# Kernel optimization log

Hardware: AMD Instinct MI355X
Metric: run time of the kernel (lower is better)

## Reference

```python
import jax, jax.numpy as jnp
import numpy as np

EPS = 1e-6
R = 8


def _gram_schmidt(U, eps=EPS):
    # Modified Gram-Schmidt over the r columns of U (dim, r), matching the
    # sequential projection loop in HouseholderReflection.get_orthogonal_matrix.
    cols = []
    u0 = U[:, 0]
    cols.append(u0 / (jnp.linalg.norm(u0) + eps))
    r = U.shape[1]
    for i in range(1, r):
        ui = U[:, i]
        for j in range(i):
            ui = ui - jnp.dot(cols[j], ui) * cols[j]
        cols.append(ui / (jnp.linalg.norm(ui) + eps))
    return cols  # list of r unit vectors (dim,)


def _orthogonal_matrix(hra_u, eps=EPS):
    # Q = prod_i (I - 2 u_i u_i^T), applied as rank-1 updates: Q <- Q - 2 (Q u) u^T
    dim = hra_u.shape[0]
    cols = _gram_schmidt(hra_u, eps)
    Q = jnp.eye(dim, dtype=hra_u.dtype)
    for u in cols:
        Q = Q - 2.0 * jnp.outer(Q @ u, u)
    return Q  # (dim, dim)


def setup_inputs() -> dict:
    key = jax.random.key(0)
    k1, k2, k3, k4, k5 = jax.random.split(key, 5)
    N, D_IN, D_HID, D_OUT = 4096, 2048, 8192, 2048
    x = jax.random.normal(k1, (N, D_IN), dtype=jnp.float32)
    hra_u = jax.random.normal(k2, (D_IN, R), dtype=jnp.float32)
    W_random = jax.random.normal(k3, (D_IN, D_HID), dtype=jnp.float32) / np.sqrt(D_IN)
    W_out = jax.random.normal(k4, (D_HID, D_OUT), dtype=jnp.float32) / np.sqrt(D_HID)
    bias = jax.random.normal(k5, (D_OUT,), dtype=jnp.float32)
    return {"x": x, "hra_u": hra_u, "W_random": W_random, "W_out": W_out, "bias": bias}


def reference(x, hra_u, W_random, W_out, bias):
    # y = gelu(x @ (Q @ W_random)) @ W_out + bias  (torch nn.GELU = exact erf gelu)
    Q = _orthogonal_matrix(hra_u)
    W_t = Q @ W_random                      # (D_IN, D_HID)
    h = jax.nn.gelu(x @ W_t, approximate=False)  # (N, D_HID)
    return h @ W_out + bias                 # (N, D_OUT)
```

## Files before the change

### kernel.cpp

```cpp
#include <hip/hip_runtime.h>
#include <hip/hip_bf16.h>

typedef __bf16 bf16;
typedef __bf16 bf16x4 __attribute__((ext_vector_type(4)));
typedef __bf16 bf16x8 __attribute__((ext_vector_type(8)));
typedef float  f32x4  __attribute__((ext_vector_type(4)));

#define GAS __attribute__((address_space(1)))
#define LAS __attribute__((address_space(3)))

#define NROWS 4096
#define DIN   2048
#define DHID  8192
#define DOUT  2048

__device__ __forceinline__ void gload16(const void* g, void* l) {
    __builtin_amdgcn_global_load_lds((GAS void*)g, (LAS void*)l, 16, 0, 0);
}
template <int N> __device__ __forceinline__ void vmw() {
    asm volatile("s_waitcnt vmcnt(%0)" :: "n"(N));
}
__device__ __forceinline__ void SB() { __builtin_amdgcn_sched_barrier(0); }

__global__ __launch_bounds__(64) void gs_kernel(const float* __restrict__ U,
                                                float* __restrict__ Vt) {
    __shared__ float Vs[8][DIN];
    const int l = threadIdx.x;
    float u[32];
    for (int r = 0; r < 8; ++r) {
        #pragma unroll
        for (int s = 0; s < 32; ++s) u[s] = U[(size_t)(l * 32 + s) * 8 + r];
        for (int j = 0; j < r; ++j) {
            float d = 0.f;
            #pragma unroll
            for (int s = 0; s < 32; ++s) d += Vs[j][l * 32 + s] * u[s];
            #pragma unroll
            for (int o = 32; o >= 1; o >>= 1) d += __shfl_xor(d, o);
            #pragma unroll
            for (int s = 0; s < 32; ++s) u[s] -= d * Vs[j][l * 32 + s];
        }
        float nr = 0.f;
        #pragma unroll
        for (int s = 0; s < 32; ++s) nr += u[s] * u[s];
        #pragma unroll
        for (int o = 32; o >= 1; o >>= 1) nr += __shfl_xor(nr, o);
        const float inv = 1.f / (sqrtf(nr) + 1e-6f);
        #pragma unroll
        for (int s = 0; s < 32; ++s) {
            float v = u[s] * inv;
            Vs[r][l * 32 + s] = v;
            Vt[r * DIN + l * 32 + s] = v;
        }
        __syncthreads();
    }
}

__global__ __launch_bounds__(256) void p_kernel(const float* __restrict__ W,
                                                const float* __restrict__ Vt,
                                                float* __restrict__ P) {
    const int t = threadIdx.x;
    const int c = blockIdx.x * 32 + (t & 31);
    const int part = t >> 5;
    float acc[8] = {};
    const int i0 = part * 256;
    #pragma unroll 4
    for (int i = i0; i < i0 + 256; ++i) {
        float w = W[(size_t)i * DHID + c];
        #pragma unroll
        for (int r = 0; r < 8; ++r) acc[r] = fmaf(Vt[r * DIN + i], w, acc[r]);
    }
    __shared__ float red[8][8][32];
    #pragma unroll
    for (int r = 0; r < 8; ++r) red[part][r][t & 31] = acc[r];
    __syncthreads();
    {
        int r = t >> 5, cc = t & 31;
        float s = 0.f;
        #pragma unroll
        for (int p = 0; p < 8; ++p) s += red[p][r][cc];
        P[(size_t)r * DHID + blockIdx.x * 32 + cc] = s;
    }
}

__global__ __launch_bounds__(256) void xv_kernel(const float* __restrict__ x,
                                                 const float* __restrict__ Vt,
                                                 float* __restrict__ xV,
                                                 bf16* __restrict__ xb) {
    const int row = blockIdx.x * 4 + (threadIdx.x >> 6);
    const int l = threadIdx.x & 63;
    const float* xr = x + (size_t)row * DIN;
    bf16* xbr = xb + (size_t)row * DIN;
    float acc[8] = {};
    #pragma unroll
    for (int s = 0; s < 8; ++s) {
        const int c0 = (s * 64 + l) * 4;
        float4 v = *(const float4*)&xr[c0];
        bf16x4 o = { (bf16)v.x, (bf16)v.y, (bf16)v.z, (bf16)v.w };
        *(bf16x4*)&xbr[c0] = o;
        #pragma unroll
        for (int r = 0; r < 8; ++r) {
            float4 vt = *(const float4*)&Vt[r * DIN + c0];
            acc[r] = fmaf(v.x, vt.x, fmaf(v.y, vt.y, fmaf(v.z, vt.z, fmaf(v.w, vt.w, acc[r]))));
        }
    }
    #pragma unroll
    for (int r = 0; r < 8; ++r) {
        float d = acc[r];
        #pragma unroll
        for (int o = 32; o >= 1; o >>= 1) d += __shfl_xor(d, o);
        if (l == 0) xV[(size_t)row * 8 + r] = d;
    }
}

__global__ __launch_bounds__(256) void tconv_kernel(const float* __restrict__ in,
                                                    bf16* __restrict__ out,
                                                    int R, int C) {
    __shared__ bf16 tile[64][66];
    const int t = threadIdx.x;
    const int n0 = blockIdx.x * 64, k0 = blockIdx.y * 64;
    const int rr = t >> 4, c4 = (t & 15) * 4;
    #pragma unroll
    for (int q = 0; q < 4; ++q) {
        int row = k0 + rr + q * 16;
        float4 v = *(const float4*)&in[(size_t)row * C + n0 + c4];
        tile[c4 + 0][rr + q * 16] = (bf16)v.x;
        tile[c4 + 1][rr + q * 16] = (bf16)v.y;
        tile[c4 + 2][rr + q * 16] = (bf16)v.z;
        tile[c4 + 3][rr + q * 16] = (bf16)v.w;
    }
    __syncthreads();
    const int n = t >> 2, kk = (t & 3) * 16;
    unsigned int w[8];
    #pragma unroll
    for (int i = 0; i < 8; ++i) w[i] = *(const unsigned int*)&tile[n][kk + i * 2];
    uint4 lo = { w[0], w[1], w[2], w[3] }, hi = { w[4], w[5], w[6], w[7] };
    uint4* dst = (uint4*)&out[(size_t)(n0 + n) * R + k0 + kk];
    dst[0] = lo;
    dst[1] = hi;
}

__global__ __launch_bounds__(256) void redk(float* __restrict__ out,
                                            const float* __restrict__ p1,
                                            const float* __restrict__ bias) {
    const size_t i = (size_t)blockIdx.x * 256 + threadIdx.x;
    float4 a = ((const float4*)out)[i];
    float4 b = ((const float4*)p1)[i];
    const int c4 = (int)(i & (DOUT / 4 - 1)) * 4;
    float4 bb = *(const float4*)&bias[c4];
    float4 r = { a.x + b.x + bb.x, a.y + b.y + bb.y,
                 a.z + b.z + bb.z, a.w + b.w + bb.w };
    ((float4*)out)[i] = r;
}

template <int CR, int CC, int EPI>
__global__ __launch_bounds__(512) void gemm4p(const bf16* __restrict__ A,
                                              const bf16* __restrict__ Bt,
                                              const int N, const int nk, const int lda,
                                              const float* __restrict__ e0,
                                              const float* __restrict__ e1,
                                              void* __restrict__ Cout) {
    __shared__ __align__(128) char lds[131072];
    const int t = threadIdx.x;
    const int wid = t >> 6, lane = t & 63;
    const int wr = wid >> 2, wc = wid & 3;
    const int lrow = lane & 15;
    const int lk2 = (lane >> 4) * 16;

    int bid = blockIdx.x, sk = 0;
    if constexpr (EPI == 2) { sk = bid & 1; bid >>= 1; }
    const int chunks_c = (N >> 8) / CC;
    const int xc = bid & 7;
    const int ii = bid >> 3;
    const int bm = (xc / chunks_c) * CR + ii / CC;
    const int bn = (xc % chunks_c) * CC + ii % CC;

    const size_t koff = (size_t)sk * nk * 64;
    const bf16* Abase = A + (size_t)bm * 256 * lda + koff;
    const bf16* Bbase = Bt + (size_t)bn * 256 * lda + koff;

    const unsigned aswz = (unsigned)(((lrow >> 1) & 3) << 4);
    const unsigned aoff0 = (unsigned)((wr * 128 + lrow) * 64 + lk2) ^ aswz;
    const unsigned boff0 = (unsigned)((wc * 64 + lrow) * 64 + lk2) ^ aswz;

    f32x4 acc[8][4] = {};

    auto STAGEQ = [&](int kt, int q) {
        const bf16* Pb = (q < 2) ? Abase : Bbase;
        const size_t kq = (size_t)kt * 64 + (size_t)(q & 1) * 32;
        char* reg = lds + (kt & 1) * 65536 + q * 16384;
        #pragma unroll
        for (int i2 = 0; i2 < 2; ++i2) {
            const int lin = i2 * 512 + t;
            const int row = lin >> 2;
            const int g = (lin & 3) ^ ((lin >> 3) & 3);
            gload16(Pb + (size_t)row * lda + kq + g * 8,
                    reg + (i2 * 512 + (t & 448)) * 16);
        }
    };

    auto PH_SYNC = [&]() {
        SB();
        __builtin_amdgcn_s_barrier();
        asm volatile("s_waitcnt lgkmcnt(0)");
        SB();
    };

    auto TILE64 = [&](int kt, bool dostage) {
        const char* bp = lds + (kt & 1) * 65536;
        bf16x8 av[4], bv[4], aw[4], av2[4], bv2[4], aw2[4];
        #pragma unroll
        for (int m = 0; m < 4; ++m) av[m] = *(const bf16x8*)(bp + aoff0 + m * 1024);
        #pragma unroll
        for (int n = 0; n < 4; ++n) bv[n] = *(const bf16x8*)(bp + 32768 + boff0 + n * 1024);
        if (dostage) STAGEQ(kt + 1, 0);
        PH_SYNC();
        __builtin_amdgcn_s_setprio(1);
        #pragma unroll
        for (int m = 0; m < 4; ++m)
            #pragma unroll
            for (int n = 0; n < 4; ++n)
                acc[m][n] = __builtin_amdgcn_mfma_f32_16x16x32_bf16(av[m], bv[n], acc[m][n], 0, 0, 0);
        __builtin_amdgcn_s_setprio(0);
        #pragma unroll
        for (int m = 0; m < 4; ++m) aw[m] = *(const bf16x8*)(bp + aoff0 + (m + 4) * 1024);
        if (dostage) { STAGEQ(kt + 1, 2); SB(); vmw<4>(); }
        else         { SB(); vmw<0>(); }
        PH_SYNC();
        __builtin_amdgcn_s_setprio(1);
        #pragma unroll
        for (int m = 0; m < 4; ++m)
            #pragma unroll
            for (int n = 0; n < 4; ++n)
                acc[m + 4][n] = __builtin_amdgcn_mfma_f32_16x16x32_bf16(aw[m], bv[n], acc[m + 4][n], 0, 0, 0);
        __builtin_amdgcn_s_setprio(0);
        #pragma unroll
        for (int m = 0; m < 4; ++m) av2[m] = *(const bf16x8*)(bp + 16384 + aoff0 + m * 1024);
        #pragma unroll
        for (int n = 0; n < 4; ++n) bv2[n] = *(const bf16x8*)(bp + 49152 + boff0 + n * 1024);
        if (dostage) STAGEQ(kt + 1, 1);
        PH_SYNC();
        __builtin_amdgcn_s_setprio(1);
        #pragma unroll
        for (int m = 0; m < 4; ++m)
            #pragma unroll
            for (int n = 0; n < 4; ++n)
                acc[m][n] = __builtin_amdgcn_mfma_f32_16x16x32_bf16(av2[m], bv2[n], acc[m][n], 0, 0, 0);
        __builtin_amdgcn_s_setprio(0);
        #pragma unroll
        for (int m = 0; m < 4; ++m) aw2[m] = *(const bf16x8*)(bp + 16384 + aoff0 + (m + 4) * 1024);
        if (dostage) { STAGEQ(kt + 1, 3); SB(); vmw<4>(); }
        PH_SYNC();
        __builtin_amdgcn_s_setprio(1);
        #pragma unroll
        for (int m = 0; m < 4; ++m)
            #pragma unroll
            for (int n = 0; n < 4; ++n)
                acc[m + 4][n] = __builtin_amdgcn_mfma_f32_16x16x32_bf16(aw2[m], bv2[n], acc[m + 4][n], 0, 0, 0);
        __builtin_amdgcn_s_setprio(0);
    };

    STAGEQ(0, 0); STAGEQ(0, 2); STAGEQ(0, 1); STAGEQ(0, 3);
    SB(); vmw<4>();
    __builtin_amdgcn_s_barrier();
    SB();

    for (int kt = 0; kt < nk - 1; ++kt) TILE64(kt, true);
    TILE64(nk - 1, false);

    const int jrow = (lane >> 4) << 2;
    if constexpr (EPI == 1) {
        SB();
        __builtin_amdgcn_s_barrier();
        SB();
        float* xVl = (float*)lds;
        float* Pl  = (float*)(lds + 8192);
        for (int idx = t; idx < 2048; idx += 512)
            xVl[idx] = e0[((size_t)bm * 256 + (idx >> 3)) * 8 + (idx & 7)];
        for (int idx = t; idx < 2048; idx += 512)
            Pl[idx] = e1[(size_t)(idx >> 8) * N + (size_t)bn * 256 + (idx & 255)];
        asm volatile("s_waitcnt lgkmcnt(0)");
        SB();
        __builtin_amdgcn_s_barrier();
        SB();
        bf16* outp = (bf16*)Cout;
        #pragma unroll
        for (int m = 0; m < 8; ++m)
            #pragma unroll
            for (int n = 0; n < 4; ++n)
                #pragma unroll
                for (int j = 0; j < 4; ++j) {
                    const int rl = wr * 128 + m * 16 + jrow + j;
                    const int cl = wc * 64 + n * 16 + lrow;
                    float v = acc[m][n][j];
                    float corr = 0.f;
                    #pragma unroll
                    for (int r = 0; r < 8; ++r)
                        corr = fmaf(xVl[rl * 8 + r], Pl[r * 256 + cl], corr);
                    v = fmaf(-2.f, corr, v);
                    v = 0.5f * v * (1.f + erff(v * 0.70710678118654752440f));
                    outp[((size_t)bm * 256 + rl) * N + bn * 256 + cl] = (bf16)v;
                }
    } else {
        float* outp = sk ? const_cast<float*>(e1) : (float*)Cout;
        #pragma unroll
        for (int m = 0; m < 8; ++m)
            #pragma unroll
            for (int n = 0; n < 4; ++n)
                #pragma unroll
                for (int j = 0; j < 4; ++j) {
                    const int rl = wr * 128 + m * 16 + jrow + j;
                    const int cl = wc * 64 + n * 16 + lrow;
                    outp[((size_t)bm * 256 + rl) * N + bn * 256 + cl] = acc[m][n][j];
                }
    }
}

extern "C" void kernel_launch(void* const* d_in, const int* in_sizes, int n_in,
                              void* d_out, int out_size, void* d_ws, size_t ws_size,
                              hipStream_t stream) {
    const float* x     = (const float*)d_in[0];
    const float* hra_u = (const float*)d_in[1];
    const float* Wr    = (const float*)d_in[2];
    const float* Wo    = (const float*)d_in[3];
    const float* bias  = (const float*)d_in[4];
    float* out = (float*)d_out;
    char* ws = (char*)d_ws;

    float* Vt  = (float*)(ws + 0);
    float* P   = (float*)(ws + 65536);
    float* xV  = (float*)(ws + 327680);
    bf16*  xb  = (bf16*)(ws + 458752);
    bf16*  WrT = (bf16*)(ws + 17235968);
    bf16*  WoT = (bf16*)(ws + 50790400);
    bf16*  hb  = (bf16*)(ws + 84344832);
    float* p1  = (float*)(ws + 458752);

    gs_kernel<<<dim3(1), dim3(64), 0, stream>>>(hra_u, Vt);
    p_kernel<<<dim3(DHID / 32), dim3(256), 0, stream>>>(Wr, Vt, P);
    xv_kernel<<<dim3(NROWS / 4), dim3(256), 0, stream>>>(x, Vt, xV, xb);
    tconv_kernel<<<dim3(DHID / 64, DIN / 64), dim3(256), 0, stream>>>(Wr, WrT, DIN, DHID);
    tconv_kernel<<<dim3(DOUT / 64, DHID / 64), dim3(256), 0, stream>>>(Wo, WoT, DHID, DOUT);

    gemm4p<8, 8, 1><<<dim3(512), dim3(512), 0, stream>>>(
        xb, WrT, DHID, DIN / 64, DIN, xV, P, (void*)hb);
    gemm4p<4, 4, 2><<<dim3(256), dim3(512), 0, stream>>>(
        hb, WoT, DOUT, DHID / 128, DHID, nullptr, p1, (void*)out);
    redk<<<dim3((NROWS * DOUT) / 1024), dim3(256), 0, stream>>>(out, p1, bias);
}
```

Measured before the change: 573.1 us.

## Restage GEMM prefetch in A/B half-pairs and drop sched barriers

Result: slower. 601.5 us (+5.0%).

```diff
diff --git a/kernel.cpp b/kernel.cpp
--- a/kernel.cpp
+++ b/kernel.cpp
@@ -20,7 +20,6 @@
 template <int N> __device__ __forceinline__ void vmw() {
     asm volatile("s_waitcnt vmcnt(%0)" :: "n"(N));
 }
-__device__ __forceinline__ void SB() { __builtin_amdgcn_sched_barrier(0); }
 
 __global__ __launch_bounds__(64) void gs_kernel(const float* __restrict__ U,
                                                 float* __restrict__ Vt) {
@@ -197,13 +196,7 @@
                     reg + (i2 * 512 + (t & 448)) * 16);
         }
     };
-
-    auto PH_SYNC = [&]() {
-        SB();
-        __builtin_amdgcn_s_barrier();
-        asm volatile("s_waitcnt lgkmcnt(0)");
-        SB();
-    };
+    auto STAGE2 = [&](int kt, int kh) { STAGEQ(kt, kh); STAGEQ(kt, 2 + kh); };
 
     auto TILE64 = [&](int kt, bool dostage) {
         const char* bp = lds + (kt & 1) * 65536;
@@ -212,8 +205,9 @@
         for (int m = 0; m < 4; ++m) av[m] = *(const bf16x8*)(bp + aoff0 + m * 1024);
         #pragma unroll
         for (int n = 0; n < 4; ++n) bv[n] = *(const bf16x8*)(bp + 32768 + boff0 + n * 1024);
-        if (dostage) STAGEQ(kt + 1, 0);
-        PH_SYNC();
+        if (dostage) STAGE2(kt + 1, 0);
+        __builtin_amdgcn_s_barrier();
+        asm volatile("s_waitcnt lgkmcnt(0)");
         __builtin_amdgcn_s_setprio(1);
         #pragma unroll
         for (int m = 0; m < 4; ++m)
@@ -221,11 +215,13 @@
             for (int n = 0; n < 4; ++n)
                 acc[m][n] = __builtin_amdgcn_mfma_f32_16x16x32_bf16(av[m], bv[n], acc[m][n], 0, 0, 0);
         __builtin_amdgcn_s_setprio(0);
+        __builtin_amdgcn_s_barrier();
         #pragma unroll
         for (int m = 0; m < 4; ++m) aw[m] = *(const bf16x8*)(bp + aoff0 + (m + 4) * 1024);
-        if (dostage) { STAGEQ(kt + 1, 2); SB(); vmw<4>(); }
-        else         { SB(); vmw<0>(); }
-        PH_SYNC();
+        if (dostage) { STAGE2(kt + 1, 1); vmw<8>(); }
+        else         { vmw<0>(); }
+        __builtin_amdgcn_s_barrier();
+        asm volatile("s_waitcnt lgkmcnt(0)");
         __builtin_amdgcn_s_setprio(1);
         #pragma unroll
         for (int m = 0; m < 4; ++m)
@@ -233,12 +229,13 @@
             for (int n = 0; n < 4; ++n)
                 acc[m + 4][n] = __builtin_amdgcn_mfma_f32_16x16x32_bf16(aw[m], bv[n], acc[m + 4][n], 0, 0, 0);
         __builtin_amdgcn_s_setprio(0);
+        __builtin_amdgcn_s_barrier();
         #pragma unroll
         for (int m = 0; m < 4; ++m) av2[m] = *(const bf16x8*)(bp + 16384 + aoff0 + m * 1024);
         #pragma unroll
         for (int n = 0; n < 4; ++n) bv2[n] = *(const bf16x8*)(bp + 49152 + boff0 + n * 1024);
-        if (dostage) STAGEQ(kt + 1, 1);
-        PH_SYNC();
+        __builtin_amdgcn_s_barrier();
+        asm volatile("s_waitcnt lgkmcnt(0)");
         __builtin_amdgcn_s_setprio(1);
         #pragma unroll
         for (int m = 0; m < 4; ++m)
@@ -246,10 +243,12 @@
             for (int n = 0; n < 4; ++n)
                 acc[m][n] = __builtin_amdgcn_mfma_f32_16x16x32_bf16(av2[m], bv2[n], acc[m][n], 0, 0, 0);
         __builtin_amdgcn_s_setprio(0);
+        __builtin_amdgcn_s_barrier();
         #pragma unroll
         for (int m = 0; m < 4; ++m) aw2[m] = *(const bf16x8*)(bp + 16384 + aoff0 + (m + 4) * 1024);
-        if (dostage) { STAGEQ(kt + 1, 3); SB(); vmw<4>(); }
-        PH_SYNC();
+        if (dostage) vmw<4>();
+        __builtin_amdgcn_s_barrier();
+        asm volatile("s_waitcnt lgkmcnt(0)");
         __builtin_amdgcn_s_setprio(1);
         #pragma unroll
         for (int m = 0; m < 4; ++m)
@@ -257,31 +256,25 @@
             for (int n = 0; n < 4; ++n)
                 acc[m + 4][n] = __builtin_amdgcn_mfma_f32_16x16x32_bf16(aw2[m], bv2[n], acc[m + 4][n], 0, 0, 0);
         __builtin_amdgcn_s_setprio(0);
+        __builtin_amdgcn_s_barrier();
     };
 
-    STAGEQ(0, 0); STAGEQ(0, 2); STAGEQ(0, 1); STAGEQ(0, 3);
-    SB(); vmw<4>();
+    STAGE2(0, 0); STAGE2(0, 1);
+    vmw<4>();
     __builtin_amdgcn_s_barrier();
-    SB();
 
     for (int kt = 0; kt < nk - 1; ++kt) TILE64(kt, true);
     TILE64(nk - 1, false);
 
     const int jrow = (lane >> 4) << 2;
     if constexpr (EPI == 1) {
-        SB();
-        __builtin_amdgcn_s_barrier();
-        SB();
         float* xVl = (float*)lds;
         float* Pl  = (float*)(lds + 8192);
         for (int idx = t; idx < 2048; idx += 512)
             xVl[idx] = e0[((size_t)bm * 256 + (idx >> 3)) * 8 + (idx & 7)];
         for (int idx = t; idx < 2048; idx += 512)
             Pl[idx] = e1[(size_t)(idx >> 8) * N + (size_t)bn * 256 + (idx & 255)];
-        asm volatile("s_waitcnt lgkmcnt(0)");
-        SB();
-        __builtin_amdgcn_s_barrier();
-        SB();
+        __syncthreads();
         bf16* outp = (bf16*)Cout;
         #pragma unroll
         for (int m = 0; m < 8; ++m)
```
